# Kernel optimization log

Measured on AMD Instinct MI355X. Metric: run time of the kernel, lower is better.

The kernel has to match this reference:

```python
import jax, jax.numpy as jnp
import numpy as np

B, D = 65536, 1024
H1, H2, OUT = 512, 256, 12
EPS = 1e-5


def setup_inputs() -> dict:
    key = jax.random.key(0)
    ks = jax.random.split(key, 8)
    x = jax.random.normal(ks[0], (B, D), dtype=jnp.float32)
    W1 = jax.random.normal(ks[1], (D, H1), dtype=jnp.float32) * (1.0 / np.sqrt(D))
    b1 = jnp.zeros((H1,), jnp.float32)
    g1 = jnp.ones((H1,), jnp.float32)
    be1 = jnp.zeros((H1,), jnp.float32)
    W2 = jax.random.normal(ks[2], (H1, H2), dtype=jnp.float32) * (1.0 / np.sqrt(H1))
    b2 = jnp.zeros((H2,), jnp.float32)
    g2 = jnp.ones((H2,), jnp.float32)
    be2 = jnp.zeros((H2,), jnp.float32)
    W3 = jax.random.normal(ks[3], (H2, OUT), dtype=jnp.float32) * (1.0 / np.sqrt(H2))
    b3 = jnp.zeros((OUT,), jnp.float32)
    return {"x": x, "W1": W1, "b1": b1, "g1": g1, "be1": be1,
            "W2": W2, "b2": b2, "g2": g2, "be2": be2, "W3": W3, "b3": b3}


def _bn(h, g, b):
    # BatchNorm1d in training mode: batch mean/var (biased), eps=1e-5
    mu = h.mean(axis=0)
    var = h.var(axis=0)
    return (h - mu) * jax.lax.rsqrt(var + EPS) * g + b


def reference(x, W1, b1, g1, be1, W2, b2, g2, be2, W3, b3):
    h = jax.nn.relu(_bn(x @ W1 + b1, g1, be1))
    h = jax.nn.relu(_bn(h @ W2 + b2, g2, be2))
    y = h @ W3 + b3                      # [B, 12]
    t = y[:, 9:].reshape(-1, 3, 1)       # translation [B,3,1]
    m = y[:, :9].reshape(-1, 3, 3)       # raw rotation [B,3,3]
    # symmetric orthogonalization (SVD-based projection onto SO(3))
    u, s, vt = jnp.linalg.svd(m, full_matrices=False)
    det = jnp.linalg.det(u @ vt)[:, None, None]
    vt_adj = jnp.concatenate([vt[:, :2, :], vt[:, 2:, :] * det], axis=1)
    r = u @ vt_adj                        # [B,3,3], det = +1
    return jnp.concatenate([r, t], axis=-1)  # [B,3,4]
```

## Files before the change

### kernel.cpp

```cpp
#include <hip/hip_runtime.h>

#define B_ROWS 65536
#define D_IN   1024
#define H1N    512
#define H2N    256

typedef _Float16 half8  __attribute__((ext_vector_type(8)));
typedef __fp16   fp16x2 __attribute__((ext_vector_type(2)));
typedef float    f32x4v __attribute__((ext_vector_type(4)));

#define GLOAD_LDS16(gp, lp) \
    __builtin_amdgcn_global_load_lds((const __attribute__((address_space(1))) void*)(gp), \
                                     (__attribute__((address_space(3))) void*)(lp), 16, 0, 0)

__global__ __launch_bounds__(256)
void splitw(const float* __restrict__ W1, const float* __restrict__ W2,
            _Float16* __restrict__ w1h, _Float16* __restrict__ w1l,
            _Float16* __restrict__ w2h, _Float16* __restrict__ w2l)
{
    int b = blockIdx.x, t = threadIdx.x;
    if (b < H1N) {
        for (int k = t; k < D_IN; k += 256) {
            float v = W1[(size_t)k * H1N + b];
            _Float16 h = (_Float16)v;
            w1h[(size_t)b * D_IN + k] = h;
            w1l[(size_t)b * D_IN + k] = (_Float16)(v - (float)h);
        }
    } else {
        int n = b - H1N;
        for (int k = t; k < H1N; k += 256) {
            float v = W2[(size_t)k * H2N + n];
            _Float16 h = (_Float16)v;
            w2h[(size_t)n * H1N + k] = h;
            w2l[(size_t)n * H1N + k] = (_Float16)(v - (float)h);
        }
    }
}

__device__ __forceinline__ void split8(f32x4v va, f32x4v vb, half8& hi, half8& lo)
{
    float v[8] = {va[0], va[1], va[2], va[3], vb[0], vb[1], vb[2], vb[3]};
    union { fp16x2 h2[4]; half8 h8; } H, L;
    #pragma unroll
    for (int i = 0; i < 4; ++i) {
        float h0 = __int_as_float(__float_as_int(v[2*i])   & 0xFFFFE000);
        float h1 = __int_as_float(__float_as_int(v[2*i+1]) & 0xFFFFE000);
        H.h2[i] = __builtin_amdgcn_cvt_pkrtz(h0, h1);
        L.h2[i] = __builtin_amdgcn_cvt_pkrtz(v[2*i] - h0, v[2*i+1] - h1);
    }
    hi = H.h8; lo = L.h8;
}

__global__ __launch_bounds__(512, 2)
void gemm1(const float* __restrict__ A, const _Float16* __restrict__ Bth,
           const _Float16* __restrict__ Btl, const float* __restrict__ bias,
           float* __restrict__ Cout, float2* __restrict__ statp)
{
    __shared__ alignas(16) char smb[131072];
    const int A0 = 0, A1 = 32768, BH0 = 65536, BH1 = 81920, BL0 = 98304, BL1 = 114688;

    const int tid = threadIdx.x;
    const int l = tid & 63;
    const int w = tid >> 6;
    const int wr = w >> 2, wc = w & 3;

    const int bid = blockIdx.x;
    const int L   = (bid & 7) * 64 + (bid >> 3);
    const int mb  = L >> 1, nb = L & 1;
    const int m0  = mb << 8, n0 = nb << 8;

    auto stage = [&](int buf, int ks) {
        #pragma unroll
        for (int i = 0; i < 4; ++i) {
            int rbase = w * 32 + i * 8;
            int r = rbase + (l >> 3);
            int c = (l & 7) ^ (r & 7);
            const float* g = A + (size_t)(m0 + r) * D_IN + ks * 32 + c * 4;
            GLOAD_LDS16(g, smb + (buf ? A1 : A0) + rbase * 128);
        }
        #pragma unroll
        for (int i = 0; i < 2; ++i) {
            int rbase = (w * 2 + i) * 16;
            int r = rbase + (l >> 2);
            int c = (l & 3) ^ ((r >> 1) & 3);
            const _Float16* gh = Bth + (size_t)(n0 + r) * D_IN + ks * 32 + c * 8;
            const _Float16* gl = Btl + (size_t)(n0 + r) * D_IN + ks * 32 + c * 8;
            GLOAD_LDS16(gh, smb + (buf ? BH1 : BH0) + rbase * 64);
            GLOAD_LDS16(gl, smb + (buf ? BL1 : BL0) + rbase * 64);
        }
    };

    f32x4v acc[8][4] = {};

    stage(0, 0);
    __syncthreads();

    #pragma unroll 2
    for (int ks = 0; ks < 32; ++ks) {
        const int buf = ks & 1;
        if (ks < 31) stage(buf ^ 1, ks + 1);

        const char* pa  = smb + (buf ? A1 : A0);
        const char* pbh = smb + (buf ? BH1 : BH0);
        const char* pbl = smb + (buf ? BL1 : BL0);

        half8 bh[4], bl[4];
        #pragma unroll
        for (int n = 0; n < 4; ++n) {
            int r = wc * 64 + n * 16 + (l & 15);
            int c = (l >> 4) ^ ((r >> 1) & 3);
            bh[n] = *(const half8*)(pbh + r * 64 + c * 16);
            bl[n] = *(const half8*)(pbl + r * 64 + c * 16);
        }
        #pragma unroll
        for (int mh = 0; mh < 2; ++mh) {
            half8 ah[4], al[4];
            #pragma unroll
            for (int mm = 0; mm < 4; ++mm) {
                int r = wr * 128 + (mh * 4 + mm) * 16 + (l & 15);
                const char* base = pa + r * 128;
                int c0 = ((l >> 4) * 2) ^ (r & 7);
                int c1 = (((l >> 4) * 2) | 1) ^ (r & 7);
                f32x4v va = *(const f32x4v*)(base + c0 * 16);
                f32x4v vb = *(const f32x4v*)(base + c1 * 16);
                split8(va, vb, ah[mm], al[mm]);
            }
            #pragma unroll
            for (int mm = 0; mm < 4; ++mm) {
                #pragma unroll
                for (int n = 0; n < 4; ++n) {
                    f32x4v t = acc[mh * 4 + mm][n];
                    t = __builtin_amdgcn_mfma_f32_16x16x32_f16(ah[mm], bh[n], t, 0, 0, 0);
                    t = __builtin_amdgcn_mfma_f32_16x16x32_f16(ah[mm], bl[n], t, 0, 0, 0);
                    t = __builtin_amdgcn_mfma_f32_16x16x32_f16(al[mm], bh[n], t, 0, 0, 0);
                    acc[mh * 4 + mm][n] = t;
                }
            }
        }
        __syncthreads();
    }

    float bv[4], s[4], q[4];
    #pragma unroll
    for (int n = 0; n < 4; ++n) {
        bv[n] = bias[n0 + wc * 64 + n * 16 + (l & 15)];
        s[n] = 0.f; q[n] = 0.f;
    }
    #pragma unroll
    for (int m = 0; m < 8; ++m) {
        int row = m0 + wr * 128 + m * 16 + ((l >> 4) << 2);
        #pragma unroll
        for (int n = 0; n < 4; ++n) {
            int col = n0 + wc * 64 + n * 16 + (l & 15);
            float* cp = Cout + (size_t)row * H1N + col;
            #pragma unroll
            for (int j = 0; j < 4; ++j) {
                float v = acc[m][n][j] + bv[n];
                cp[(size_t)j * H1N] = v;
                s[n] += v; q[n] += v * v;
            }
        }
    }
    #pragma unroll
    for (int n = 0; n < 4; ++n) {
        s[n] += __shfl_xor(s[n], 16); s[n] += __shfl_xor(s[n], 32);
        q[n] += __shfl_xor(q[n], 16); q[n] += __shfl_xor(q[n], 32);
    }
    __syncthreads();
    float2* red = (float2*)smb;
    if (wr == 1 && l < 16) {
        #pragma unroll
        for (int n = 0; n < 4; ++n) red[(wc * 4 + n) * 16 + l] = make_float2(s[n], q[n]);
    }
    __syncthreads();
    if (wr == 0 && l < 16) {
        #pragma unroll
        for (int n = 0; n < 4; ++n) {
            float2 o = red[(wc * 4 + n) * 16 + l];
            int col = n0 + wc * 64 + n * 16 + l;
            statp[(size_t)mb * H1N + col] = make_float2(s[n] + o.x, q[n] + o.y);
        }
    }
}

__global__ __launch_bounds__(512, 2)
void gemm2(const float* __restrict__ Hin, const _Float16* __restrict__ Bth,
           const _Float16* __restrict__ Btl, const float* __restrict__ bias,
           const float2* __restrict__ scsh, float* __restrict__ Cout,
           float2* __restrict__ statp)
{
    __shared__ alignas(16) char smb[135168];
    const int AH0 = 0, AH1 = 16384, AL0 = 32768, AL1 = 49152;
    const int BH0 = 65536, BH1 = 81920, BL0 = 98304, BL1 = 114688;
    float2* scl = (float2*)(smb + 131072);

    const int tid = threadIdx.x;
    const int l = tid & 63;
    const int w = tid >> 6;
    const int wr = w >> 2, wc = w & 3;

    const int bid = blockIdx.x;
    const int mb  = (bid & 7) * 32 + (bid >> 3);
    const int m0  = mb << 8;
    const int n0  = 0;

    const int ar = tid >> 1, ch = tid & 1;

    float4 rga[4];
    auto load_regs = [&](int ks) {
        const float4* p = (const float4*)(Hin + (size_t)(m0 + ar) * H1N + ks * 32 + ch * 16);
        rga[0] = p[0]; rga[1] = p[1]; rga[2] = p[2]; rga[3] = p[3];
    };
    auto stageB = [&](int buf, int ks) {
        #pragma unroll
        for (int i = 0; i < 2; ++i) {
            int rbase = (w * 2 + i) * 16;
            int r = rbase + (l >> 2);
            int c = (l & 3) ^ ((r >> 1) & 3);
            const _Float16* gh = Bth + (size_t)(n0 + r) * H1N + ks * 32 + c * 8;
            const _Float16* gl = Btl + (size_t)(n0 + r) * H1N + ks * 32 + c * 8;
            GLOAD_LDS16(gh, smb + (buf ? BH1 : BH0) + rbase * 64);
            GLOAD_LDS16(gl, smb + (buf ? BL1 : BL0) + rbase * 64);
        }
    };
    auto proc_write = [&](int buf, int ks) {
        float v[16];
        #pragma unroll
        for (int p = 0; p < 4; ++p) {
            v[p*4+0] = rga[p].x; v[p*4+1] = rga[p].y;
            v[p*4+2] = rga[p].z; v[p*4+3] = rga[p].w;
        }
        const float2* sp = scl + ks * 32 + ch * 16;
        float hm[16], lv[16];
        #pragma unroll
        for (int i = 0; i < 16; ++i) {
            float2 s2 = sp[i];
            float vv = fmaxf(fmaf(v[i], s2.x, s2.y), 0.f);
            hm[i] = __int_as_float(__float_as_int(vv) & 0xFFFFE000);
            lv[i] = vv - hm[i];
        }
        union { fp16x2 h2[4]; half8 h8; } H[2], Lo[2];
        #pragma unroll
        for (int hb = 0; hb < 2; ++hb) {
            #pragma unroll
            for (int i = 0; i < 4; ++i) {
                H[hb].h2[i]  = __builtin_amdgcn_cvt_pkrtz(hm[hb*8+2*i], hm[hb*8+2*i+1]);
                Lo[hb].h2[i] = __builtin_amdgcn_cvt_pkrtz(lv[hb*8+2*i], lv[hb*8+2*i+1]);
            }
        }
        char* bhp = smb + (buf ? AH1 : AH0) + ar * 64;
        char* blp = smb + (buf ? AL1 : AL0) + ar * 64;
        int sw = (ar >> 1) & 3;
        *(half8*)(bhp + (((ch*2)     ^ sw) * 16)) = H[0].h8;
        *(half8*)(bhp + (((ch*2 + 1) ^ sw) * 16)) = H[1].h8;
        *(half8*)(blp + (((ch*2)     ^ sw) * 16)) = Lo[0].h8;
        *(half8*)(blp + (((ch*2 + 1) ^ sw) * 16)) = Lo[1].h8;
    };

    for (int i = tid; i < H1N; i += 512) scl[i] = scsh[i];
    load_regs(0);
    stageB(0, 0);
    __syncthreads();
    proc_write(0, 0);
    __syncthreads();

    f32x4v acc[8][4] = {};
    for (int ks = 0; ks < 16; ++ks) {
        const int buf = ks & 1;
        if (ks < 15) { load_regs(ks + 1); stageB(buf ^ 1, ks + 1); }

        const char* pah = smb + (buf ? AH1 : AH0);
        const char* pal = smb + (buf ? AL1 : AL0);
        const char* pbh = smb + (buf ? BH1 : BH0);
        const char* pbl = smb + (buf ? BL1 : BL0);

        half8 bh[4], bl[4];
        #pragma unroll
        for (int n = 0; n < 4; ++n) {
            int r = wc * 64 + n * 16 + (l & 15);
            int c = (l >> 4) ^ ((r >> 1) & 3);
            bh[n] = *(const half8*)(pbh + r * 64 + c * 16);
            bl[n] = *(const half8*)(pbl + r * 64 + c * 16);
        }
        #pragma unroll
        for (int mh = 0; mh < 2; ++mh) {
            half8 ah[4], al[4];
            #pragma unroll
            for (int mm = 0; mm < 4; ++mm) {
                int r = wr * 128 + (mh * 4 + mm) * 16 + (l & 15);
                int c = (l >> 4) ^ ((r >> 1) & 3);
                ah[mm] = *(const half8*)(pah + r * 64 + c * 16);
                al[mm] = *(const half8*)(pal + r * 64 + c * 16);
            }
            #pragma unroll
            for (int mm = 0; mm < 4; ++mm) {
                #pragma unroll
                for (int n = 0; n < 4; ++n) {
                    f32x4v t = acc[mh * 4 + mm][n];
                    t = __builtin_amdgcn_mfma_f32_16x16x32_f16(ah[mm], bh[n], t, 0, 0, 0);
                    t = __builtin_amdgcn_mfma_f32_16x16x32_f16(ah[mm], bl[n], t, 0, 0, 0);
                    t = __builtin_amdgcn_mfma_f32_16x16x32_f16(al[mm], bh[n], t, 0, 0, 0);
                    acc[mh * 4 + mm][n] = t;
                }
            }
        }
        if (ks < 15) proc_write(buf ^ 1, ks + 1);
        __syncthreads();
    }

    float bv[4], s[4], q[4];
    #pragma unroll
    for (int n = 0; n < 4; ++n) {
        bv[n] = bias[n0 + wc * 64 + n * 16 + (l & 15)];
        s[n] = 0.f; q[n] = 0.f;
    }
    #pragma unroll
    for (int m = 0; m < 8; ++m) {
        int row = m0 + wr * 128 + m * 16 + ((l >> 4) << 2);
        #pragma unroll
        for (int n = 0; n < 4; ++n) {
            int col = n0 + wc * 64 + n * 16 + (l & 15);
            float* cp = Cout + (size_t)row * H2N + col;
            #pragma unroll
            for (int j = 0; j < 4; ++j) {
                float v = acc[m][n][j] + bv[n];
                cp[(size_t)j * H2N] = v;
                s[n] += v; q[n] += v * v;
            }
        }
    }
    #pragma unroll
    for (int n = 0; n < 4; ++n) {
        s[n] += __shfl_xor(s[n], 16); s[n] += __shfl_xor(s[n], 32);
        q[n] += __shfl_xor(q[n], 16); q[n] += __shfl_xor(q[n], 32);
    }
    __syncthreads();
    float2* red = (float2*)smb;
    if (wr == 1 && l < 16) {
        #pragma unroll
        for (int n = 0; n < 4; ++n) red[(wc * 4 + n) * 16 + l] = make_float2(s[n], q[n]);
    }
    __syncthreads();
    if (wr == 0 && l < 16) {
        #pragma unroll
        for (int n = 0; n < 4; ++n) {
            float2 o = red[(wc * 4 + n) * 16 + l];
            int col = n0 + wc * 64 + n * 16 + l;
            statp[(size_t)mb * H2N + col] = make_float2(s[n] + o.x, q[n] + o.y);
        }
    }
}

__global__ void reduce_stats_g(const float2* __restrict__ part, int nparts, int ncols,
                               const float* __restrict__ g, const float* __restrict__ be,
                               float2* __restrict__ scsh)
{
    int c = blockIdx.x * blockDim.x + threadIdx.x;
    if (c >= ncols) return;
    float s = 0.f, q = 0.f;
    for (int p = 0; p < nparts; ++p) {
        float2 v = part[(size_t)p * ncols + c];
        s += v.x; q += v.y;
    }
    const float invB = 1.f / 65536.f;
    float mu = s * invB, var = q * invB - mu * mu;
    float sc = g[c] * rsqrtf(var + 1e-5f);
    scsh[c] = make_float2(sc, be[c] - mu * sc);
}

__device__ __forceinline__ void jrot(float A[3][3], float V[3][3], int p, int q)
{
    float apq = A[p][q];
    float tau = A[q][q] - A[p][p];
    float a2  = 2.f * apq;
    float Dd  = fabsf(tau) + sqrtf(tau * tau + a2 * a2) + 1e-38f;
    float tt  = copysignf(1.f, tau) * a2 / Dd;
    float c   = 1.f / sqrtf(1.f + tt * tt);
    float s   = tt * c;
    int   r   = 3 - p - q;
    float App = A[p][p], Aqq = A[q][q];
    A[p][p] = App - tt * apq;
    A[q][q] = Aqq + tt * apq;
    A[p][q] = 0.f; A[q][p] = 0.f;
    float Arp = A[r][p], Arq = A[r][q];
    A[r][p] = c * Arp - s * Arq; A[p][r] = A[r][p];
    A[r][q] = s * Arp + c * Arq; A[q][r] = A[r][q];
    #pragma unroll
    for (int i = 0; i < 3; ++i) {
        float vp = V[i][p], vq = V[i][q];
        V[i][p] = c * vp - s * vq;
        V[i][q] = s * vp + c * vq;
    }
}

__global__ __launch_bounds__(256)
void head_svd(const float* __restrict__ H2, const float2* __restrict__ scsh2,
              const float* __restrict__ W3, const float* __restrict__ b3,
              float* __restrict__ out)
{
    __shared__ alignas(16) float  w3s[H2N * 12];
    __shared__ alignas(16) float2 ss[H2N];
    __shared__ float b3s[12];
    __shared__ alignas(16) float tile[64][257];

    const int t = threadIdx.x;
    for (int i = t; i < H2N * 12; i += 256) w3s[i] = W3[i];
    ss[t] = scsh2[t];
    if (t < 12) b3s[t] = b3[t];
    __syncthreads();

    const size_t rbase = (size_t)blockIdx.x * 256;
    const size_t row = rbase + t;
    float y[12];
    #pragma unroll
    for (int o = 0; o < 12; ++o) y[o] = b3s[o];

    for (int kc = 0; kc < 4; ++kc) {
        #pragma unroll
        for (int i = 0; i < 16; ++i) {
            int rr = (t >> 4) + i * 16;
            int k4 = (t & 15) * 4;
            float4 v = *(const float4*)(H2 + (rbase + rr) * H2N + kc * 64 + k4);
            float2 sA = ss[kc*64 + k4 + 0];
            float2 sB = ss[kc*64 + k4 + 1];
            float2 sC = ss[kc*64 + k4 + 2];
            float2 sD = ss[kc*64 + k4 + 3];
            tile[k4+0][rr] = fmaxf(fmaf(v.x, sA.x, sA.y), 0.f);
            tile[k4+1][rr] = fmaxf(fmaf(v.y, sB.x, sB.y), 0.f);
            tile[k4+2][rr] = fmaxf(fmaf(v.z, sC.x, sC.y), 0.f);
            tile[k4+3][rr] = fmaxf(fmaf(v.w, sD.x, sD.y), 0.f);
        }
        __syncthreads();
        #pragma unroll 4
        for (int k = 0; k < 64; ++k) {
            float v = tile[k][t];
            const float* wp = &w3s[(kc * 64 + k) * 12];
            #pragma unroll
            for (int o = 0; o < 12; ++o) y[o] = fmaf(v, wp[o], y[o]);
        }
        __syncthreads();
    }

    float mm[3][3];
    #pragma unroll
    for (int i = 0; i < 3; ++i)
        #pragma unroll
        for (int j = 0; j < 3; ++j) mm[i][j] = y[i * 3 + j];

    float Am[3][3];
    #pragma unroll
    for (int i = 0; i < 3; ++i)
        #pragma unroll
        for (int j = 0; j < 3; ++j)
            Am[i][j] = mm[0][i]*mm[0][j] + mm[1][i]*mm[1][j] + mm[2][i]*mm[2][j];

    float V[3][3] = {{1,0,0},{0,1,0},{0,0,1}};
    #pragma unroll
    for (int sweep = 0; sweep < 5; ++sweep) {
        jrot(Am, V, 0, 1);
        jrot(Am, V, 0, 2);
        jrot(Am, V, 1, 2);
    }
    float lam0 = Am[0][0], lam1 = Am[1][1], lam2 = Am[2][2];
    if (lam0 < lam1) { float tl=lam0; lam0=lam1; lam1=tl;
        #pragma unroll
        for (int i=0;i<3;++i){float tv=V[i][0];V[i][0]=V[i][1];V[i][1]=tv;} }
    if (lam0 < lam2) { float tl=lam0; lam0=lam2; lam2=tl;
        #pragma unroll
        for (int i=0;i<3;++i){float tv=V[i][0];V[i][0]=V[i][2];V[i][2]=tv;} }
    if (lam1 < lam2) { float tl=lam1; lam1=lam2; lam2=tl;
        #pragma unroll
        for (int i=0;i<3;++i){float tv=V[i][1];V[i][1]=V[i][2];V[i][2]=tv;} }

    float det =
          V[0][0]*(V[1][1]*V[2][2]-V[1][2]*V[2][1])
        - V[0][1]*(V[1][0]*V[2][2]-V[1][2]*V[2][0])
        + V[0][2]*(V[1][0]*V[2][1]-V[1][1]*V[2][0]);
    if (det < 0.f) { V[0][2] = -V[0][2]; V[1][2] = -V[1][2]; V[2][2] = -V[2][2]; }

    float u0[3], u1[3], u2[3];
    #pragma unroll
    for (int i = 0; i < 3; ++i)
        u0[i] = mm[i][0]*V[0][0] + mm[i][1]*V[1][0] + mm[i][2]*V[2][0];
    float nn0 = 1.f / sqrtf(u0[0]*u0[0] + u0[1]*u0[1] + u0[2]*u0[2] + 1e-30f);
    u0[0]*=nn0; u0[1]*=nn0; u0[2]*=nn0;
    #pragma unroll
    for (int i = 0; i < 3; ++i)
        u1[i] = mm[i][0]*V[0][1] + mm[i][1]*V[1][1] + mm[i][2]*V[2][1];
    float d01 = u0[0]*u1[0] + u0[1]*u1[1] + u0[2]*u1[2];
    u1[0]-=d01*u0[0]; u1[1]-=d01*u0[1]; u1[2]-=d01*u0[2];
    float nn1 = 1.f / sqrtf(u1[0]*u1[0] + u1[1]*u1[1] + u1[2]*u1[2] + 1e-30f);
    u1[0]*=nn1; u1[1]*=nn1; u1[2]*=nn1;
    u2[0] = u0[1]*u1[2] - u0[2]*u1[1];
    u2[1] = u0[2]*u1[0] - u0[0]*u1[2];
    u2[2] = u0[0]*u1[1] - u0[1]*u1[0];

    float* op = out + row * 12;
    #pragma unroll
    for (int i = 0; i < 3; ++i) {
        #pragma unroll
        for (int j = 0; j < 3; ++j)
            op[i*4 + j] = u0[i]*V[j][0] + u1[i]*V[j][1] + u2[i]*V[j][2];
        op[i*4 + 3] = y[9 + i];
    }
}

extern "C" void kernel_launch(void* const* d_in, const int* in_sizes, int n_in,
                              void* d_out, int out_size, void* d_ws, size_t ws_size,
                              hipStream_t stream)
{
    (void)in_sizes; (void)n_in; (void)out_size; (void)ws_size;

    const float* x   = (const float*)d_in[0];
    const float* W1  = (const float*)d_in[1];
    const float* b1  = (const float*)d_in[2];
    const float* g1  = (const float*)d_in[3];
    const float* be1 = (const float*)d_in[4];
    const float* W2  = (const float*)d_in[5];
    const float* b2  = (const float*)d_in[6];
    const float* g2  = (const float*)d_in[7];
    const float* be2 = (const float*)d_in[8];
    const float* W3  = (const float*)d_in[9];
    const float* b3  = (const float*)d_in[10];
    float* out = (float*)d_out;

    char* ws = (char*)d_ws;
    size_t off = 0;
    auto take = [&](size_t bytes) -> void* {
        void* p = ws + off;
        off += (bytes + 255) & ~(size_t)255;
        return p;
    };
    _Float16* w1h = (_Float16*)take((size_t)H1N * D_IN * 2);
    _Float16* w1l = (_Float16*)take((size_t)H1N * D_IN * 2);
    _Float16* w2h = (_Float16*)take((size_t)H2N * H1N * 2);
    _Float16* w2l = (_Float16*)take((size_t)H2N * H1N * 2);
    float*  h1    = (float*) take((size_t)B_ROWS * H1N * 4);
    float*  h2    = (float*) take((size_t)B_ROWS * H2N * 4);
    float2* part1 = (float2*)take((size_t)256 * H1N * 8);
    float2* part2 = (float2*)take((size_t)256 * H2N * 8);
    float2* scsh1 = (float2*)take((size_t)H1N * 8);
    float2* scsh2 = (float2*)take((size_t)H2N * 8);

    splitw<<<dim3(H1N + H2N), dim3(256), 0, stream>>>(W1, W2, w1h, w1l, w2h, w2l);

    gemm1<<<dim3(512), dim3(512), 0, stream>>>(x, w1h, w1l, b1, h1, part1);
    reduce_stats_g<<<dim3(2), dim3(256), 0, stream>>>(part1, 256, H1N, g1, be1, scsh1);

    gemm2<<<dim3(256), dim3(512), 0, stream>>>(h1, w2h, w2l, b2, scsh1, h2, part2);
    reduce_stats_g<<<dim3(1), dim3(256), 0, stream>>>(part2, 256, H2N, g2, be2, scsh2);

    head_svd<<<dim3(B_ROWS / 256), dim3(256), 0, stream>>>(h2, scsh2, W3, b3, out);
}
```

Before: 415.3 us.

## Unify GEMMs into one template that splits A once into fp16 hi/lo in LDS

Measured after the change: 411.5 us. No clear change (-0.9%).

```diff
diff --git a/kernel.cpp b/kernel.cpp
--- a/kernel.cpp
+++ b/kernel.cpp
@@ -14,50 +14,56 @@
                                      (__attribute__((address_space(3))) void*)(lp), 16, 0, 0)
 
 __global__ __launch_bounds__(256)
-void splitw(const float* __restrict__ W1, const float* __restrict__ W2,
-            _Float16* __restrict__ w1h, _Float16* __restrict__ w1l,
-            _Float16* __restrict__ w2h, _Float16* __restrict__ w2l)
-{
-    int b = blockIdx.x, t = threadIdx.x;
-    if (b < H1N) {
-        for (int k = t; k < D_IN; k += 256) {
-            float v = W1[(size_t)k * H1N + b];
-            _Float16 h = (_Float16)v;
-            w1h[(size_t)b * D_IN + k] = h;
-            w1l[(size_t)b * D_IN + k] = (_Float16)(v - (float)h);
-        }
-    } else {
-        int n = b - H1N;
-        for (int k = t; k < H1N; k += 256) {
-            float v = W2[(size_t)k * H2N + n];
-            _Float16 h = (_Float16)v;
-            w2h[(size_t)n * H1N + k] = h;
-            w2l[(size_t)n * H1N + k] = (_Float16)(v - (float)h);
-        }
-    }
-}
-
-__device__ __forceinline__ void split8(f32x4v va, f32x4v vb, half8& hi, half8& lo)
-{
-    float v[8] = {va[0], va[1], va[2], va[3], vb[0], vb[1], vb[2], vb[3]};
-    union { fp16x2 h2[4]; half8 h8; } H, L;
-    #pragma unroll
-    for (int i = 0; i < 4; ++i) {
-        float h0 = __int_as_float(__float_as_int(v[2*i])   & 0xFFFFE000);
-        float h1 = __int_as_float(__float_as_int(v[2*i+1]) & 0xFFFFE000);
-        H.h2[i] = __builtin_amdgcn_cvt_pkrtz(h0, h1);
-        L.h2[i] = __builtin_amdgcn_cvt_pkrtz(v[2*i] - h0, v[2*i+1] - h1);
-    }
-    hi = H.h8; lo = L.h8;
-}
-
+void splitw_t(const float* __restrict__ W, _Float16* __restrict__ wh,
+              _Float16* __restrict__ wl, int Kd, int Nd)
+{
+    __shared__ float tile[64][65];
+    const int t = threadIdx.x;
+    const int ntn = Nd >> 6;
+    const int k0 = (blockIdx.x / ntn) << 6;
+    const int n0 = (blockIdx.x % ntn) << 6;
+
+    {
+        int r = t >> 4, c4 = (t & 15) << 2;
+        #pragma unroll
+        for (int i = 0; i < 4; ++i) {
+            float4 v = *(const float4*)(W + (size_t)(k0 + r + i * 16) * Nd + n0 + c4);
+            tile[r + i*16][c4+0] = v.x; tile[r + i*16][c4+1] = v.y;
+            tile[r + i*16][c4+2] = v.z; tile[r + i*16][c4+3] = v.w;
+        }
+    }
+    __syncthreads();
+    {
+        int n = t >> 2, kc = (t & 3) << 4;
+        union { fp16x2 h2[8]; half8 h8[2]; } H, L;
+        #pragma unroll
+        for (int i = 0; i < 8; ++i) {
+            float v0 = tile[kc + 2*i][n], v1 = tile[kc + 2*i + 1][n];
+            float h0 = __int_as_float(__float_as_int(v0) & 0xFFFFE000);
+            float h1 = __int_as_float(__float_as_int(v1) & 0xFFFFE000);
+            H.h2[i] = __builtin_amdgcn_cvt_pkrtz(h0, h1);
+            L.h2[i] = __builtin_amdgcn_cvt_pkrtz(v0 - h0, v1 - h1);
+        }
+        _Float16* ph = wh + (size_t)(n0 + n) * Kd + k0 + kc;
+        _Float16* pl = wl + (size_t)(n0 + n) * Kd + k0 + kc;
+        *(half8*)ph = H.h8[0]; *(half8*)(ph + 8) = H.h8[1];
+        *(half8*)pl = L.h8[0]; *(half8*)(pl + 8) = L.h8[1];
+    }
+}
+
+template<int K, int NB, bool BNRELU>
 __global__ __launch_bounds__(512, 2)
-void gemm1(const float* __restrict__ A, const _Float16* __restrict__ Bth,
-           const _Float16* __restrict__ Btl, const float* __restrict__ bias,
-           float* __restrict__ Cout, float2* __restrict__ statp)
-{
-    __shared__ alignas(16) char smb[131072];
-    const int A0 = 0, A1 = 32768, BH0 = 65536, BH1 = 81920, BL0 = 98304, BL1 = 114688;
+void gemm_fused(const float* __restrict__ Ain, const _Float16* __restrict__ Bth,
+                const _Float16* __restrict__ Btl, const float* __restrict__ bias,
+                const float2* __restrict__ scsh, float* __restrict__ Cout,
+                float2* __restrict__ statp)
+{
+    constexpr int N  = NB * 256;
+    constexpr int NS = K / 32;
+    __shared__ alignas(16) char smb[131072 + 4096];
+    const int AH0 = 0,     AH1 = 16384, AL0 = 32768, AL1 = 49152;
+    const int BH0 = 65536, BH1 = 81920, BL0 = 98304, BL1 = 114688;
+    float2* scl = (float2*)(smb + 131072);
 
     const int tid = threadIdx.x;
     const int l = tid & 63;
@@ -65,42 +71,86 @@
     const int wr = w >> 2, wc = w & 3;
 
     const int bid = blockIdx.x;
-    const int L   = (bid & 7) * 64 + (bid >> 3);
-    const int mb  = L >> 1, nb = L & 1;
-    const int m0  = mb << 8, n0 = nb << 8;
-
-    auto stage = [&](int buf, int ks) {
-        #pragma unroll
-        for (int i = 0; i < 4; ++i) {
-            int rbase = w * 32 + i * 8;
-            int r = rbase + (l >> 3);
-            int c = (l & 7) ^ (r & 7);
-            const float* g = A + (size_t)(m0 + r) * D_IN + ks * 32 + c * 4;
-            GLOAD_LDS16(g, smb + (buf ? A1 : A0) + rbase * 128);
-        }
+    constexpr int CPX = 32 * NB;
+    const int L  = (bid & 7) * CPX + (bid >> 3);
+    const int mb = L / NB, nb = L % NB;
+    const int m0 = mb << 8, n0 = nb << 8;
+
+    const int ar = tid >> 1, ch = tid & 1;
+
+    if constexpr (BNRELU) {
+        for (int i = tid; i < K; i += 512) scl[i] = scsh[i];
+    }
+    (void)scsh;
+
+    float4 rga[4];
+    auto load_regs = [&](int ks) {
+        const float4* p = (const float4*)(Ain + (size_t)(m0 + ar) * K + ks * 32 + ch * 16);
+        rga[0] = p[0]; rga[1] = p[1]; rga[2] = p[2]; rga[3] = p[3];
+    };
+
+    auto stageB = [&](int buf, int ks) {
         #pragma unroll
         for (int i = 0; i < 2; ++i) {
             int rbase = (w * 2 + i) * 16;
             int r = rbase + (l >> 2);
             int c = (l & 3) ^ ((r >> 1) & 3);
-            const _Float16* gh = Bth + (size_t)(n0 + r) * D_IN + ks * 32 + c * 8;
-            const _Float16* gl = Btl + (size_t)(n0 + r) * D_IN + ks * 32 + c * 8;
+            const _Float16* gh = Bth + (size_t)(n0 + r) * K + ks * 32 + c * 8;
+            const _Float16* gl = Btl + (size_t)(n0 + r) * K + ks * 32 + c * 8;
             GLOAD_LDS16(gh, smb + (buf ? BH1 : BH0) + rbase * 64);
             GLOAD_LDS16(gl, smb + (buf ? BL1 : BL0) + rbase * 64);
         }
     };
 
+    auto proc_write = [&](int buf, int ks) {
+        float v[16];
+        #pragma unroll
+        for (int p = 0; p < 4; ++p) {
+            v[p*4+0] = rga[p].x; v[p*4+1] = rga[p].y;
+            v[p*4+2] = rga[p].z; v[p*4+3] = rga[p].w;
+        }
+        if constexpr (BNRELU) {
+            const float2* sp = scl + ks * 32 + ch * 16;
+            #pragma unroll
+            for (int i = 0; i < 16; ++i) {
+                float2 s2 = sp[i];
+                v[i] = fmaxf(fmaf(v[i], s2.x, s2.y), 0.f);
+            }
+        }
+        union { fp16x2 h2[4]; half8 h8; } H[2], Lo[2];
+        #pragma unroll
+        for (int hb = 0; hb < 2; ++hb) {
+            #pragma unroll
+            for (int i = 0; i < 4; ++i) {
+                float v0 = v[hb*8 + 2*i], v1 = v[hb*8 + 2*i + 1];
+                float h0 = __int_as_float(__float_as_int(v0) & 0xFFFFE000);
+                float h1 = __int_as_float(__float_as_int(v1) & 0xFFFFE000);
+                H[hb].h2[i]  = __builtin_amdgcn_cvt_pkrtz(h0, h1);
+                Lo[hb].h2[i] = __builtin_amdgcn_cvt_pkrtz(v0 - h0, v1 - h1);
+            }
+        }
+        char* bhp = smb + (buf ? AH1 : AH0) + ar * 64;
+        char* blp = smb + (buf ? AL1 : AL0) + ar * 64;
+        int sw = (ar >> 1) & 3;
+        *(half8*)(bhp + (((ch*2)     ^ sw) * 16)) = H[0].h8;
+        *(half8*)(bhp + (((ch*2 + 1) ^ sw) * 16)) = H[1].h8;
+        *(half8*)(blp + (((ch*2)     ^ sw) * 16)) = Lo[0].h8;
+        *(half8*)(blp + (((ch*2 + 1) ^ sw) * 16)) = Lo[1].h8;
+    };
+
+    load_regs(0);
+    stageB(0, 0);
+    __syncthreads();
+    proc_write(0, 0);
+    __syncthreads();
+
     f32x4v acc[8][4] = {};
-
-    stage(0, 0);
-    __syncthreads();
-
-    #pragma unroll 2
-    for (int ks = 0; ks < 32; ++ks) {
+    for (int ks = 0; ks < NS; ++ks) {
         const int buf = ks & 1;
-        if (ks < 31) stage(buf ^ 1, ks + 1);
-
-        const char* pa  = smb + (buf ? A1 : A0);
+        if (ks < NS - 1) { load_regs(ks + 1); stageB(buf ^ 1, ks + 1); }
+
+        const char* pah = smb + (buf ? AH1 : AH0);
+        const char* pal = smb + (buf ? AL1 : AL0);
         const char* pbh = smb + (buf ? BH1 : BH0);
         const char* pbl = smb + (buf ? BL1 : BL0);
 
@@ -118,12 +168,9 @@
             #pragma unroll
             for (int mm = 0; mm < 4; ++mm) {
                 int r = wr * 128 + (mh * 4 + mm) * 16 + (l & 15);
-                const char* base = pa + r * 128;
-                int c0 = ((l >> 4) * 2) ^ (r & 7);
-                int c1 = (((l >> 4) * 2) | 1) ^ (r & 7);
-                f32x4v va = *(const f32x4v*)(base + c0 * 16);
-                f32x4v vb = *(const f32x4v*)(base + c1 * 16);
-                split8(va, vb, ah[mm], al[mm]);
+                int c = (l >> 4) ^ ((r >> 1) & 3);
+                ah[mm] = *(const half8*)(pah + r * 64 + c * 16);
+                al[mm] = *(const half8*)(pal + r * 64 + c * 16);
             }
             #pragma unroll
             for (int mm = 0; mm < 4; ++mm) {
@@ -137,6 +184,7 @@
                 }
             }
         }
+        if (ks < NS - 1) proc_write(buf ^ 1, ks + 1);
         __syncthreads();
     }
 
@@ -152,11 +200,11 @@
         #pragma unroll
         for (int n = 0; n < 4; ++n) {
             int col = n0 + wc * 64 + n * 16 + (l & 15);
-            float* cp = Cout + (size_t)row * H1N + col;
+            float* cp = Cout + (size_t)row * N + col;
             #pragma unroll
             for (int j = 0; j < 4; ++j) {
                 float v = acc[m][n][j] + bv[n];
-                cp[(size_t)j * H1N] = v;
+                cp[(size_t)j * N] = v;
                 s[n] += v; q[n] += v * v;
             }
         }
@@ -178,175 +226,7 @@
         for (int n = 0; n < 4; ++n) {
             float2 o = red[(wc * 4 + n) * 16 + l];
             int col = n0 + wc * 64 + n * 16 + l;
-            statp[(size_t)mb * H1N + col] = make_float2(s[n] + o.x, q[n] + o.y);
-        }
-    }
-}
-
-__global__ __launch_bounds__(512, 2)
-void gemm2(const float* __restrict__ Hin, const _Float16* __restrict__ Bth,
-           const _Float16* __restrict__ Btl, const float* __restrict__ bias,
-           const float2* __restrict__ scsh, float* __restrict__ Cout,
-           float2* __restrict__ statp)
-{
-    __shared__ alignas(16) char smb[135168];
-    const int AH0 = 0, AH1 = 16384, AL0 = 32768, AL1 = 49152;
-    const int BH0 = 65536, BH1 = 81920, BL0 = 98304, BL1 = 114688;
-    float2* scl = (float2*)(smb + 131072);
-
-    const int tid = threadIdx.x;
-    const int l = tid & 63;
-    const int w = tid >> 6;
-    const int wr = w >> 2, wc = w & 3;
-
-    const int bid = blockIdx.x;
-    const int mb  = (bid & 7) * 32 + (bid >> 3);
-    const int m0  = mb << 8;
-    const int n0  = 0;
-
-    const int ar = tid >> 1, ch = tid & 1;
-
-    float4 rga[4];
-    auto load_regs = [&](int ks) {
-        const float4* p = (const float4*)(Hin + (size_t)(m0 + ar) * H1N + ks * 32 + ch * 16);
-        rga[0] = p[0]; rga[1] = p[1]; rga[2] = p[2]; rga[3] = p[3];
-    };
-    auto stageB = [&](int buf, int ks) {
-        #pragma unroll
-        for (int i = 0; i < 2; ++i) {
-            int rbase = (w * 2 + i) * 16;
-            int r = rbase + (l >> 2);
-            int c = (l & 3) ^ ((r >> 1) & 3);
-            const _Float16* gh = Bth + (size_t)(n0 + r) * H1N + ks * 32 + c * 8;
-            const _Float16* gl = Btl + (size_t)(n0 + r) * H1N + ks * 32 + c * 8;
-            GLOAD_LDS16(gh, smb + (buf ? BH1 : BH0) + rbase * 64);
-            GLOAD_LDS16(gl, smb + (buf ? BL1 : BL0) + rbase * 64);
-        }
-    };
-    auto proc_write = [&](int buf, int ks) {
-        float v[16];
-        #pragma unroll
-        for (int p = 0; p < 4; ++p) {
-            v[p*4+0] = rga[p].x; v[p*4+1] = rga[p].y;
-            v[p*4+2] = rga[p].z; v[p*4+3] = rga[p].w;
-        }
-        const float2* sp = scl + ks * 32 + ch * 16;
-        float hm[16], lv[16];
-        #pragma unroll
-        for (int i = 0; i < 16; ++i) {
-            float2 s2 = sp[i];
-            float vv = fmaxf(fmaf(v[i], s2.x, s2.y), 0.f);
-            hm[i] = __int_as_float(__float_as_int(vv) & 0xFFFFE000);
-            lv[i] = vv - hm[i];
-        }
-        union { fp16x2 h2[4]; half8 h8; } H[2], Lo[2];
-        #pragma unroll
-        for (int hb = 0; hb < 2; ++hb) {
-            #pragma unroll
-            for (int i = 0; i < 4; ++i) {
-                H[hb].h2[i]  = __builtin_amdgcn_cvt_pkrtz(hm[hb*8+2*i], hm[hb*8+2*i+1]);
-                Lo[hb].h2[i] = __builtin_amdgcn_cvt_pkrtz(lv[hb*8+2*i], lv[hb*8+2*i+1]);
-            }
-        }
-        char* bhp = smb + (buf ? AH1 : AH0) + ar * 64;
-        char* blp = smb + (buf ? AL1 : AL0) + ar * 64;
-        int sw = (ar >> 1) & 3;
-        *(half8*)(bhp + (((ch*2)     ^ sw) * 16)) = H[0].h8;
-        *(half8*)(bhp + (((ch*2 + 1) ^ sw) * 16)) = H[1].h8;
-        *(half8*)(blp + (((ch*2)     ^ sw) * 16)) = Lo[0].h8;
-        *(half8*)(blp + (((ch*2 + 1) ^ sw) * 16)) = Lo[1].h8;
-    };
-
-    for (int i = tid; i < H1N; i += 512) scl[i] = scsh[i];
-    load_regs(0);
-    stageB(0, 0);
-    __syncthreads();
-    proc_write(0, 0);
-    __syncthreads();
-
-    f32x4v acc[8][4] = {};
-    for (int ks = 0; ks < 16; ++ks) {
-        const int buf = ks & 1;
-        if (ks < 15) { load_regs(ks + 1); stageB(buf ^ 1, ks + 1); }
-
-        const char* pah = smb + (buf ? AH1 : AH0);
-        const char* pal = smb + (buf ? AL1 : AL0);
-        const char* pbh = smb + (buf ? BH1 : BH0);
-        const char* pbl = smb + (buf ? BL1 : BL0);
-
-        half8 bh[4], bl[4];
-        #pragma unroll
-        for (int n = 0; n < 4; ++n) {
-            int r = wc * 64 + n * 16 + (l & 15);
-            int c = (l >> 4) ^ ((r >> 1) & 3);
-            bh[n] = *(const half8*)(pbh + r * 64 + c * 16);
-            bl[n] = *(const half8*)(pbl + r * 64 + c * 16);
-        }
-        #pragma unroll
-        for (int mh = 0; mh < 2; ++mh) {
-            half8 ah[4], al[4];
-            #pragma unroll
-            for (int mm = 0; mm < 4; ++mm) {
-                int r = wr * 128 + (mh * 4 + mm) * 16 + (l & 15);
-                int c = (l >> 4) ^ ((r >> 1) & 3);
-                ah[mm] = *(const half8*)(pah + r * 64 + c * 16);
-                al[mm] = *(const half8*)(pal + r * 64 + c * 16);
-            }
-            #pragma unroll
-            for (int mm = 0; mm < 4; ++mm) {
-                #pragma unroll
-                for (int n = 0; n < 4; ++n) {
-                    f32x4v t = acc[mh * 4 + mm][n];
-                    t = __builtin_amdgcn_mfma_f32_16x16x32_f16(ah[mm], bh[n], t, 0, 0, 0);
-                    t = __builtin_amdgcn_mfma_f32_16x16x32_f16(ah[mm], bl[n], t, 0, 0, 0);
-                    t = __builtin_amdgcn_mfma_f32_16x16x32_f16(al[mm], bh[n], t, 0, 0, 0);
-                    acc[mh * 4 + mm][n] = t;
-                }
-            }
-        }
-        if (ks < 15) proc_write(buf ^ 1, ks + 1);
-        __syncthreads();
-    }
-
-    float bv[4], s[4], q[4];
-    #pragma unroll
-    for (int n = 0; n < 4; ++n) {
-        bv[n] = bias[n0 + wc * 64 + n * 16 + (l & 15)];
-        s[n] = 0.f; q[n] = 0.f;
-    }
-    #pragma unroll
-    for (int m = 0; m < 8; ++m) {
-        int row = m0 + wr * 128 + m * 16 + ((l >> 4) << 2);
-        #pragma unroll
-        for (int n = 0; n < 4; ++n) {
-            int col = n0 + wc * 64 + n * 16 + (l & 15);
-            float* cp = Cout + (size_t)row * H2N + col;
-            #pragma unroll
-            for (int j = 0; j < 4; ++j) {
-                float v = acc[m][n][j] + bv[n];
-                cp[(size_t)j * H2N] = v;
-                s[n] += v; q[n] += v * v;
-            }
-        }
-    }
-    #pragma unroll
-    for (int n = 0; n < 4; ++n) {
-        s[n] += __shfl_xor(s[n], 16); s[n] += __shfl_xor(s[n], 32);
-        q[n] += __shfl_xor(q[n], 16); q[n] += __shfl_xor(q[n], 32);
-    }
-    __syncthreads();
-    float2* red = (float2*)smb;
-    if (wr == 1 && l < 16) {
-        #pragma unroll
-        for (int n = 0; n < 4; ++n) red[(wc * 4 + n) * 16 + l] = make_float2(s[n], q[n]);
-    }
-    __syncthreads();
-    if (wr == 0 && l < 16) {
-        #pragma unroll
-        for (int n = 0; n < 4; ++n) {
-            float2 o = red[(wc * 4 + n) * 16 + l];
-            int col = n0 + wc * 64 + n * 16 + l;
-            statp[(size_t)mb * H2N + col] = make_float2(s[n] + o.x, q[n] + o.y);
+            statp[(size_t)mb * N + col] = make_float2(s[n] + o.x, q[n] + o.y);
         }
     }
 }
@@ -542,12 +422,15 @@
     float2* scsh1 = (float2*)take((size_t)H1N * 8);
     float2* scsh2 = (float2*)take((size_t)H2N * 8);
 
-    splitw<<<dim3(H1N + H2N), dim3(256), 0, stream>>>(W1, W2, w1h, w1l, w2h, w2l);
-
-    gemm1<<<dim3(512), dim3(512), 0, stream>>>(x, w1h, w1l, b1, h1, part1);
+    splitw_t<<<dim3((D_IN/64) * (H1N/64)), dim3(256), 0, stream>>>(W1, w1h, w1l, D_IN, H1N);
+    splitw_t<<<dim3((H1N/64) * (H2N/64)), dim3(256), 0, stream>>>(W2, w2h, w2l, H1N, H2N);
+
+    gemm_fused<D_IN, 2, false><<<dim3(512), dim3(512), 0, stream>>>(
+        x, w1h, w1l, b1, nullptr, h1, part1);
     reduce_stats_g<<<dim3(2), dim3(256), 0, stream>>>(part1, 256, H1N, g1, be1, scsh1);
 
-    gemm2<<<dim3(256), dim3(512), 0, stream>>>(h1, w2h, w2l, b2, scsh1, h2, part2);
+    gemm_fused<H1N, 1, true><<<dim3(256), dim3(512), 0, stream>>>(
+        h1, w2h, w2l, b2, scsh1, h2, part2);
     reduce_stats_g<<<dim3(1), dim3(256), 0, stream>>>(part2, 256, H2N, g2, be2, scsh2);
 
     head_svd<<<dim3(B_ROWS / 256), dim3(256), 0, stream>>>(h2, scsh2, W3, b3, out);
```
